# Kernel tuning notes

Hardware: AMD Instinct MI355X
Metric: run time of the kernel (lower is better)

Reference implementation:

```python
import jax, jax.numpy as jnp
import numpy as np

ALPHA = 0.2
NEG_INF = -1e10


def setup_inputs() -> dict:
    key = jax.random.key(0)
    k1, k2, k3, k4 = jax.random.split(key, 4)
    N, Fin, H, Fout = 4096, 512, 8, 64
    x = jax.random.normal(k1, (N, Fin), dtype=jnp.float32)
    adj = jax.random.randint(k2, (N, N), 0, 2, dtype=jnp.int32)
    W = jax.random.normal(k3, (Fin, H * Fout), dtype=jnp.float32) * (1.0 / np.sqrt(Fin))
    a = jax.random.normal(k4, (2 * Fout, 1), dtype=jnp.float32) * (1.0 / np.sqrt(2 * Fout))
    return {"x": x, "adj": adj, "W": W, "a": a}


def reference(x, adj, W, a):
    N = x.shape[0]
    Fout2 = a.shape[0]          # 2 * out_features
    Fout = Fout2 // 2
    Wh = (x @ W).reshape(N, -1, Fout)          # [N, H, F]
    H = Wh.shape[1]
    # Additive attention decomposes: e[i,j,h] = leakyrelu(a1.Wh[i,h] + a2.Wh[j,h]).
    # This is the exact same math as concatenating [Wh_i; Wh_j] and matmul with a,
    # without materializing the N*N*H*2F tensor.
    a1, a2 = a[:Fout, 0], a[Fout:, 0]
    f1 = jnp.einsum('nhf,f->nh', Wh, a1)       # [N, H]
    f2 = jnp.einsum('nhf,f->nh', Wh, a2)       # [N, H]
    e = jax.nn.leaky_relu(f1[:, None, :] + f2[None, :, :], negative_slope=ALPHA)  # [N, N, H]
    e = jnp.where(adj[:, :, None] > 0, e, NEG_INF)
    attention = jax.nn.softmax(e, axis=1)      # softmax over neighbors j (dim=1)
    # dropout p=0.0 (eval-mode determinism)
    # h_prime[h] = attention[h] @ Wh[h]; then mean over heads
    h_prime = jnp.einsum('ijh,jhf->if', attention, Wh) / H  # [N, F]
    return h_prime
```

## Files before the change

### kernel.cpp

```cpp
#include <hip/hip_runtime.h>

#define LRELU_ALPHA 0.2f

constexpr int NN    = 4096;
constexpr int FIN   = 512;
constexpr int NH    = 8;
constexpr int FOUT  = 64;
constexpr int NFLAT = NH * FOUT;
constexpr float LOG2E = 1.4426950408889634f;

typedef __attribute__((ext_vector_type(8))) __bf16 bf16x8;
typedef __attribute__((ext_vector_type(4))) __bf16 bf16x4;
typedef __attribute__((ext_vector_type(4))) float f32x4;
typedef __attribute__((ext_vector_type(16))) float f32x16;

__device__ __forceinline__ unsigned bitsmear(unsigned mk, int e) {
    return (unsigned)(((int)(mk << (31 - e))) >> 31);
}

__global__ __launch_bounds__(256) void k_prep(const float* __restrict__ W,
                                              __bf16* __restrict__ wtsw) {
    __shared__ float tile[64][68];
    const int bid = blockIdx.x;
    const int t = threadIdx.x;
    const int kt = bid >> 3;
    const int fb = (bid & 7) * 64;
    {
        const int kk = t >> 2, cq = (t & 3) * 16;
        #pragma unroll
        for (int i = 0; i < 4; ++i)
            *(float4*)&tile[kk][cq + i * 4] =
                *(const float4*)&W[(size_t)(kt * 64 + kk) * NFLAT + fb + cq + i * 4];
    }
    __syncthreads();
    const int fl = t >> 2;
    #pragma unroll
    for (int c = 0; c < 2; ++c) {
        int gs = (t & 3) * 2 + c;
        int g  = gs ^ (fl & 7);
        bf16x8 o;
        #pragma unroll
        for (int jo = 0; jo < 8; ++jo) o[jo] = (__bf16)tile[g * 8 + jo][fl];
        *(bf16x8*)&wtsw[((size_t)(kt * NFLAT + fb + fl)) * 64 + gs * 8] = o;
    }
}

__global__ __launch_bounds__(256) void k_main(const float* __restrict__ x,
                                              const int* __restrict__ adj,
                                              const float* __restrict__ av,
                                              const __bf16* __restrict__ wtsw,
                                              __bf16* __restrict__ whtB32,
                                              float* __restrict__ f1T,
                                              float* __restrict__ f2pn,
                                              unsigned long long* __restrict__ bmT) {
    __shared__ alignas(16) __bf16 Bs[2][64 * 64];
    const int bid = blockIdx.x;
    const int t = threadIdx.x;
    if (bid < 512) {
        const int wv = t >> 6, l = t & 63;
        const int jt = bid & 63, h = bid >> 6;
        const int bm = jt * 64, bn = h * 64;
        const int lm = l & 15, lk = l >> 4;
        const int swB = (lm & 7) << 4;

        f32x4 acc[4] = {};
        auto stageB = [&](int kt, int bb) {
            #pragma unroll
            for (int kq = 0; kq < 2; ++kq) {
                int u = t + kq * 256;
                __builtin_amdgcn_global_load_lds(
                    (const __attribute__((address_space(1))) void*)(wtsw + (size_t)(kt * NFLAT + bn) * 64 + u * 8),
                    (__attribute__((address_space(3))) void*)((char*)&Bs[bb][0] + u * 16), 16, 0, 0);
            }
        };

        stageB(0, 0);
        const float* xrow = &x[(size_t)(bm + wv * 16 + lm) * FIN + lk * 8];
        for (int kt = 0; kt < 8; ++kt) {
            bf16x8 aF[2];
            #pragma unroll
            for (int ks = 0; ks < 2; ++ks) {
                float4 u0 = *(const float4*)&xrow[kt * 64 + ks * 32];
                float4 u1 = *(const float4*)&xrow[kt * 64 + ks * 32 + 4];
                bf16x8 af;
                af[0] = (__bf16)u0.x; af[1] = (__bf16)u0.y; af[2] = (__bf16)u0.z; af[3] = (__bf16)u0.w;
                af[4] = (__bf16)u1.x; af[5] = (__bf16)u1.y; af[6] = (__bf16)u1.z; af[7] = (__bf16)u1.w;
                aF[ks] = af;
            }
            __syncthreads();
            if (kt < 7) stageB(kt + 1, (kt + 1) & 1);
            const char* wb = (const char*)&Bs[kt & 1][0];
            #pragma unroll
            for (int q = 0; q < 4; ++q) {
                #pragma unroll
                for (int ks = 0; ks < 2; ++ks) {
                    bf16x8 bF = *(const bf16x8*)(wb + (((q * 16 + lm) * 128 + lk * 16 + ks * 64) ^ swB));
                    acc[q] = __builtin_amdgcn_mfma_f32_16x16x32_bf16(aF[ks], bF, acc[q], 0, 0, 0);
                }
            }
        }
        {
            char* blk = (char*)whtB32 + ((size_t)(h * 64 + jt) << 13);
            const int jg = wv * 2 + (lk >> 1);
            const int j7o = (lk & 1) * 8;
            #pragma unroll
            for (int q = 0; q < 4; ++q) {
                const int f = q * 16 + lm;
                bf16x4 o;
                #pragma unroll
                for (int r = 0; r < 4; ++r) o[r] = (__bf16)acc[q][r];
                *(bf16x4*)(blk + (jg * 64 + f) * 16 + j7o) = o;
            }
        }
        float av1[4], av2[4];
        #pragma unroll
        for (int q = 0; q < 4; ++q) {
            av1[q] = av[q * 16 + lm];
            av2[q] = av[64 + q * 16 + lm];
        }
        float s1[4] = {}, s2[4] = {};
        #pragma unroll
        for (int q = 0; q < 4; ++q)
            #pragma unroll
            for (int r = 0; r < 4; ++r) {
                s1[r] = fmaf(acc[q][r], av1[q], s1[r]);
                s2[r] = fmaf(acc[q][r], av2[q], s2[r]);
            }
        #pragma unroll
        for (int off = 1; off < 16; off <<= 1) {
            #pragma unroll
            for (int r = 0; r < 4; ++r) {
                s1[r] += __shfl_xor(s1[r], off);
                s2[r] += __shfl_xor(s2[r], off);
            }
        }
        if (lm == 0) {
            #pragma unroll
            for (int r = 0; r < 4; ++r) {
                const int io = bm + wv * 16 + lk * 4 + r;
                f1T[h * NN + io] = s1[r] * LOG2E;
                float s2l = s2[r] * LOG2E;
                float2 v = make_float2(exp2f(s2l), exp2f(LRELU_ALPHA * s2l));
                *(float2*)&f2pn[2 * ((size_t)h * NN + io)] = v;
            }
        }
    } else {
        const size_t base = (size_t)(bid - 512) * 16384;
        for (int it = 0; it < 64; ++it) {
            size_t idx = base + (size_t)it * 256 + t;
            int v = adj[idx];
            unsigned long long b = __ballot(v > 0);
            if ((t & 63) == 0) {
                int i = (int)(idx >> 12);
                int jt = (int)((idx >> 6) & 63);
                bmT[(size_t)jt * NN + i] = b;
            }
        }
    }
}

__global__ __launch_bounds__(256, 2) void k_attn(const unsigned long long* __restrict__ bmT,
                                                 const __bf16* __restrict__ whtB32,
                                                 const float* __restrict__ f1T,
                                                 const float* __restrict__ f2pn,
                                                 float* __restrict__ oacc) {
    __shared__ alignas(16) char Ws[4][2][8192];

    const int t   = threadIdx.x;
    const int wv  = t >> 6, l = t & 63;
    const int gi0 = blockIdx.x * 32;
    const int h   = blockIdx.y;
    const int jt0 = wv * 16;

    const int lc = l & 31, hi = l >> 5;
    const int iA = gi0 + lc;
    const float f1v = f1T[h * NN + iA];
    const float E1p = exp2f(f1v);
    const float E1n = exp2f(LRELU_ALPHA * f1v);

    f32x16 acc0 = {}, acc1 = {};
    float lpart = 0.f;

    const char* gsrc = (const char*)whtB32 + ((size_t)(h * 64 + jt0) << 13) + l * 16;
    const char* fptr = (const char*)f2pn + ((size_t)h * NN + (size_t)jt0 * 64) * 8 + hi * 64;
    const unsigned long long* mptr = bmT + (size_t)jt0 * NN + iA;
    char* const wsA = &Ws[wv][0][0];
    char* const wsB = &Ws[wv][1][0];
    const int dsoff = (hi << 10) | (lc << 4);

    auto stage = [&](const char* src, char* dstbase) {
        #pragma unroll
        for (int k = 0; k < 8; ++k)
            __builtin_amdgcn_global_load_lds(
                (const __attribute__((address_space(1))) void*)(src + k * 1024),
                (__attribute__((address_space(3))) void*)(dstbase + l * 16 + k * 1024), 16, 0, 0);
    };
    auto loadF2 = [&](float4* F, const char* fp) {
        #pragma unroll
        for (int js = 0; js < 4; ++js)
            #pragma unroll
            for (int u = 0; u < 4; ++u)
                F[js * 4 + u] = *(const float4*)(fp + js * 128 + u * 16);
    };
    auto compute = [&](const char* wsb, const float4* F, unsigned long long m) {
        const unsigned long long ml = m >> (hi * 8);
        const char* bp = wsb + dsoff;
        #pragma unroll
        for (int js = 0; js < 4; ++js) {
            unsigned mk = (unsigned)(ml >> (16 * js));
            bf16x8 aF;
            #pragma unroll
            for (int u = 0; u < 4; ++u) {
                float4 vv = F[js * 4 + u];
                float a0 = fmaxf(E1p * vv.x, E1n * vv.y);
                float a1 = fmaxf(E1p * vv.z, E1n * vv.w);
                a0 = __uint_as_float(__float_as_uint(a0) & bitsmear(mk, 2 * u));
                a1 = __uint_as_float(__float_as_uint(a1) & bitsmear(mk, 2 * u + 1));
                lpart += a0 + a1;
                aF[2 * u]     = (__bf16)a0;
                aF[2 * u + 1] = (__bf16)a1;
            }
            bf16x8 bF0 = *(const bf16x8*)(bp + js * 2048);
            bf16x8 bF1 = *(const bf16x8*)(bp + js * 2048 + 512);
            __builtin_amdgcn_s_setprio(1);
            acc0 = __builtin_amdgcn_mfma_f32_32x32x16_bf16(aF, bF0, acc0, 0, 0, 0);
            acc1 = __builtin_amdgcn_mfma_f32_32x32x16_bf16(aF, bF1, acc1, 0, 0, 0);
            __builtin_amdgcn_s_setprio(0);
        }
    };

    float4 fA[16], fB[16];
    unsigned long long mA_, mB_;

    stage(gsrc, wsA);
    __builtin_amdgcn_sched_barrier(0);
    loadF2(fA, fptr);
    mA_ = *mptr;
    __builtin_amdgcn_sched_barrier(0);
    gsrc += 8192; fptr += 512; mptr += NN;

    #pragma unroll 1
    for (int jj = 0; jj < 16; jj += 2) {
        stage(gsrc, wsB);
        __builtin_amdgcn_sched_barrier(0);
        loadF2(fB, fptr);
        mB_ = *mptr;
        __builtin_amdgcn_sched_barrier(0);
        gsrc += 8192; fptr += 512; mptr += NN;
        asm volatile("s_waitcnt vmcnt(25)" ::: "memory");
        __builtin_amdgcn_sched_barrier(0);
        compute(wsA, fA, mA_);
        stage(gsrc, wsA);
        __builtin_amdgcn_sched_barrier(0);
        loadF2(fA, fptr);
        mA_ = *mptr;
        __builtin_amdgcn_sched_barrier(0);
        gsrc += 8192; fptr += 512; mptr += NN;
        asm volatile("s_waitcnt vmcnt(25)" ::: "memory");
        __builtin_amdgcn_sched_barrier(0);
        compute(wsB, fB, mB_);
    }

    asm volatile("s_waitcnt vmcnt(0)" ::: "memory");
    __builtin_amdgcn_sched_barrier(0);

    {
        float* Rp = (float*)wsA;
        float* Lp = (float*)wsB;
        #pragma unroll
        for (int reg = 0; reg < 16; ++reg) {
            const int row = (reg & 3) + 8 * (reg >> 2) + 4 * hi;
            Rp[row * 64 + lc]      = acc0[reg];
            Rp[row * 64 + 32 + lc] = acc1[reg];
        }
        Lp[hi * 32 + lc] = lpart;
    }
    __syncthreads();

    {
        const int row = t >> 3, c0 = (t & 7) * 8;
        float ls = 0.f;
        #pragma unroll
        for (int w2 = 0; w2 < 4; ++w2) {
            const float* Lp2 = (const float*)&Ws[w2][1][0];
            ls += Lp2[row] + Lp2[32 + row];
        }
        const float inv = 1.0f / (ls * (float)NH);
        f32x4 s0 = {}, s1 = {};
        #pragma unroll
        for (int w2 = 0; w2 < 4; ++w2) {
            const float* Rp2 = (const float*)&Ws[w2][0][0];
            s0 += *(const f32x4*)&Rp2[row * 64 + c0];
            s1 += *(const f32x4*)&Rp2[row * 64 + c0 + 4];
        }
        float* dst = &oacc[(size_t)(gi0 + row) * NFLAT + h * 64 + c0];
        *(f32x4*)dst       = s0 * inv;
        *(f32x4*)(dst + 4) = s1 * inv;
    }
}

__global__ __launch_bounds__(256) void k_norm(const float* __restrict__ oacc,
                                              float* __restrict__ out) {
    int t = blockIdx.x * 256 + threadIdx.x;
    int i = t >> 4, fq = (t & 15) * 4;
    f32x4 s = {};
    #pragma unroll
    for (int h = 0; h < 8; ++h)
        s += *(const f32x4*)&oacc[(size_t)i * NFLAT + h * 64 + fq];
    *(f32x4*)&out[(size_t)i * FOUT + fq] = s;
}

extern "C" void kernel_launch(void* const* d_in, const int* in_sizes, int n_in,
                              void* d_out, int out_size, void* d_ws, size_t ws_size,
                              hipStream_t stream) {
    const float* x   = (const float*)d_in[0];
    const int*   adj = (const int*)d_in[1];
    const float* W   = (const float*)d_in[2];
    const float* a   = (const float*)d_in[3];
    float* out = (float*)d_out;

    char* ws = (char*)d_ws;
    float* oacc = (float*)ws;           ws += (size_t)NN * NFLAT * 4;
    float* f1T = (float*)ws;            ws += (size_t)NH * NN * 4;
    float* f2pn = (float*)ws;           ws += (size_t)NH * NN * 8;
    __bf16* whtB32 = (__bf16*)ws;       ws += (size_t)NFLAT * NN * 2;
    unsigned long long* bmT = (unsigned long long*)ws; ws += (size_t)NN * NN / 8;
    __bf16* wtsw = (__bf16*)ws;         ws += (size_t)FIN * NFLAT * 2;

    k_prep<<<64, 256, 0, stream>>>(W, wtsw);
    k_main<<<1536, 256, 0, stream>>>(x, adj, a, wtsw, whtB32, f1T, f2pn, bmT);
    k_attn<<<dim3(NN / 32, NH), 256, 0, stream>>>(bmT, whtB32, f1T, f2pn, oacc);
    k_norm<<<NN * FOUT / 4 / 256, 256, 0, stream>>>(oacc, out);
}
```

Before: 101.7 us.

## Halve attention stage tiles to fit four blocks per CU

The per-wave LDS staging buffers and the register-held f2 arrays in the attention kernel are cut in half. Each loop iteration now processes four half-size stages, and the adjacency bitmask word is reused across two consecutive half-stages. The row-sum partials move to a small dedicated shared array. Launch bounds rise from 2 to 4 blocks per CU, so the whole grid can be resident at once. The cost is more loop iterations and waitcnt points per unit of work, shallower prefetch per stage, and tighter register limits that could cause spills.

```diff
diff --git a/kernel.cpp b/kernel.cpp
--- a/kernel.cpp
+++ b/kernel.cpp
@@ -159,12 +159,13 @@
     }
 }
 
-__global__ __launch_bounds__(256, 2) void k_attn(const unsigned long long* __restrict__ bmT,
+__global__ __launch_bounds__(256, 4) void k_attn(const unsigned long long* __restrict__ bmT,
                                                  const __bf16* __restrict__ whtB32,
                                                  const float* __restrict__ f1T,
                                                  const float* __restrict__ f2pn,
                                                  float* __restrict__ oacc) {
-    __shared__ alignas(16) char Ws[4][2][8192];
+    __shared__ alignas(16) char Ws[4][2][4096];
+    __shared__ float Lsh[4][64];
 
     const int t   = threadIdx.x;
     const int wv  = t >> 6, l = t & 63;
@@ -190,28 +191,27 @@
 
     auto stage = [&](const char* src, char* dstbase) {
         #pragma unroll
-        for (int k = 0; k < 8; ++k)
+        for (int k = 0; k < 4; ++k)
             __builtin_amdgcn_global_load_lds(
                 (const __attribute__((address_space(1))) void*)(src + k * 1024),
                 (__attribute__((address_space(3))) void*)(dstbase + l * 16 + k * 1024), 16, 0, 0);
     };
     auto loadF2 = [&](float4* F, const char* fp) {
         #pragma unroll
-        for (int js = 0; js < 4; ++js)
+        for (int js = 0; js < 2; ++js)
             #pragma unroll
             for (int u = 0; u < 4; ++u)
                 F[js * 4 + u] = *(const float4*)(fp + js * 128 + u * 16);
     };
-    auto compute = [&](const char* wsb, const float4* F, unsigned long long m) {
-        const unsigned long long ml = m >> (hi * 8);
+    auto compute = [&](const char* wsb, const float4* F, unsigned long long m, int H) {
         const char* bp = wsb + dsoff;
         #pragma unroll
-        for (int js = 0; js < 4; ++js) {
-            unsigned mk = (unsigned)(ml >> (16 * js));
+        for (int jsl = 0; jsl < 2; ++jsl) {
+            unsigned mk = (unsigned)(m >> (16 * (2 * H + jsl) + 8 * hi));
             bf16x8 aF;
             #pragma unroll
             for (int u = 0; u < 4; ++u) {
-                float4 vv = F[js * 4 + u];
+                float4 vv = F[jsl * 4 + u];
                 float a0 = fmaxf(E1p * vv.x, E1n * vv.y);
                 float a1 = fmaxf(E1p * vv.z, E1n * vv.w);
                 a0 = __uint_as_float(__float_as_uint(a0) & bitsmear(mk, 2 * u));
@@ -220,8 +220,8 @@
                 aF[2 * u]     = (__bf16)a0;
                 aF[2 * u + 1] = (__bf16)a1;
             }
-            bf16x8 bF0 = *(const bf16x8*)(bp + js * 2048);
-            bf16x8 bF1 = *(const bf16x8*)(bp + js * 2048 + 512);
+            bf16x8 bF0 = *(const bf16x8*)(bp + jsl * 2048);
+            bf16x8 bF1 = *(const bf16x8*)(bp + jsl * 2048 + 512);
             __builtin_amdgcn_s_setprio(1);
             acc0 = __builtin_amdgcn_mfma_f32_32x32x16_bf16(aF, bF0, acc0, 0, 0, 0);
             acc1 = __builtin_amdgcn_mfma_f32_32x32x16_bf16(aF, bF1, acc1, 0, 0, 0);
@@ -229,36 +229,53 @@
         }
     };
 
-    float4 fA[16], fB[16];
+    float4 fA[8], fB[8];
     unsigned long long mA_, mB_;
 
     stage(gsrc, wsA);
     __builtin_amdgcn_sched_barrier(0);
     loadF2(fA, fptr);
-    mA_ = *mptr;
+    mA_ = mptr[0];
     __builtin_amdgcn_sched_barrier(0);
-    gsrc += 8192; fptr += 512; mptr += NN;
+    gsrc += 4096; fptr += 256;
 
     #pragma unroll 1
-    for (int jj = 0; jj < 16; jj += 2) {
+    for (int tt = 0; tt < 16; tt += 2) {
         stage(gsrc, wsB);
         __builtin_amdgcn_sched_barrier(0);
         loadF2(fB, fptr);
-        mB_ = *mptr;
-        __builtin_amdgcn_sched_barrier(0);
-        gsrc += 8192; fptr += 512; mptr += NN;
-        asm volatile("s_waitcnt vmcnt(25)" ::: "memory");
-        __builtin_amdgcn_sched_barrier(0);
-        compute(wsA, fA, mA_);
+        __builtin_amdgcn_sched_barrier(0);
+        gsrc += 4096; fptr += 256;
+        asm volatile("s_waitcnt vmcnt(12)" ::: "memory");
+        __builtin_amdgcn_sched_barrier(0);
+        compute(wsA, fA, mA_, 0);
         stage(gsrc, wsA);
         __builtin_amdgcn_sched_barrier(0);
         loadF2(fA, fptr);
-        mA_ = *mptr;
-        __builtin_amdgcn_sched_barrier(0);
-        gsrc += 8192; fptr += 512; mptr += NN;
-        asm volatile("s_waitcnt vmcnt(25)" ::: "memory");
-        __builtin_amdgcn_sched_barrier(0);
-        compute(wsB, fB, mB_);
+        mB_ = mptr[NN];
+        __builtin_amdgcn_sched_barrier(0);
+        gsrc += 4096; fptr += 256;
+        asm volatile("s_waitcnt vmcnt(13)" ::: "memory");
+        __builtin_amdgcn_sched_barrier(0);
+        compute(wsB, fB, mA_, 1);
+        stage(gsrc, wsB);
+        __builtin_amdgcn_sched_barrier(0);
+        loadF2(fB, fptr);
+        __builtin_amdgcn_sched_barrier(0);
+        gsrc += 4096; fptr += 256;
+        asm volatile("s_waitcnt vmcnt(12)" ::: "memory");
+        __builtin_amdgcn_sched_barrier(0);
+        compute(wsA, fA, mB_, 0);
+        stage(gsrc, wsA);
+        __builtin_amdgcn_sched_barrier(0);
+        loadF2(fA, fptr);
+        mA_ = mptr[2 * NN];
+        __builtin_amdgcn_sched_barrier(0);
+        gsrc += 4096; fptr += 256;
+        asm volatile("s_waitcnt vmcnt(13)" ::: "memory");
+        __builtin_amdgcn_sched_barrier(0);
+        compute(wsB, fB, mB_, 1);
+        mptr += 2 * NN;
     }
 
     asm volatile("s_waitcnt vmcnt(0)" ::: "memory");
@@ -266,14 +283,13 @@
 
     {
         float* Rp = (float*)wsA;
-        float* Lp = (float*)wsB;
         #pragma unroll
         for (int reg = 0; reg < 16; ++reg) {
             const int row = (reg & 3) + 8 * (reg >> 2) + 4 * hi;
             Rp[row * 64 + lc]      = acc0[reg];
             Rp[row * 64 + 32 + lc] = acc1[reg];
         }
-        Lp[hi * 32 + lc] = lpart;
+        Lsh[wv][hi * 32 + lc] = lpart;
     }
     __syncthreads();
 
@@ -281,10 +297,8 @@
         const int row = t >> 3, c0 = (t & 7) * 8;
         float ls = 0.f;
         #pragma unroll
-        for (int w2 = 0; w2 < 4; ++w2) {
-            const float* Lp2 = (const float*)&Ws[w2][1][0];
-            ls += Lp2[row] + Lp2[32 + row];
-        }
+        for (int w2 = 0; w2 < 4; ++w2)
+            ls += Lsh[w2][row] + Lsh[w2][32 + row];
         const float inv = 1.0f / (ls * (float)NH);
         f32x4 s0 = {}, s1 = {};
         #pragma unroll
```

Result: slower. 144.7 us (+42.3%).
